# Optimization experiments

Hardware: AMD Instinct MI355X
Metric: run time of the kernel (lower is better)

Reference implementation:

```python
import jax, jax.numpy as jnp
import numpy as np

N = 400000   # active voxels
C = 64       # channels
G = 128      # voxel grid side
K = 27       # 3x3x3 kernel offsets
EPS = 1e-5   # BatchNorm eps


def _build_kernel_maps(rng):
    # random sparse 3D coordinates (unique voxels in a G^3 grid)
    lin = rng.choice(G ** 3, size=N, replace=False)
    coords = np.stack(np.unravel_index(lin, (G, G, G)), -1).astype(np.int64)  # [N,3]
    lut = np.full(G ** 3, N, dtype=np.int32)  # sentinel N = missing neighbor
    lut[lin] = np.arange(N, dtype=np.int32)
    offs = np.stack(np.meshgrid([-1, 0, 1], [-1, 0, 1], [-1, 0, 1], indexing='ij'), -1).reshape(-1, 3)  # [27,3]
    nbr = np.full((3, K, N), N, dtype=np.int32)
    for di, d in enumerate((1, 2, 3)):
        for k in range(K):
            nc = coords + offs[k] * d
            valid = np.all((nc >= 0) & (nc < G), axis=1)
            idx = np.ravel_multi_index(nc[valid].T, (G, G, G))
            nbr[di, k, valid] = lut[idx]
    return nbr


def setup_inputs() -> dict:
    key = jax.random.key(0)
    ks = jax.random.split(key, 20)
    rng = np.random.default_rng(0)
    nbr = jnp.asarray(_build_kernel_maps(rng))  # [3,27,N] int32
    s = 0.05
    inp = {
        'feats': jax.random.normal(ks[0], (N, C), jnp.float32),
        'nbr': nbr,
        # conv_init (dilation 1) + its BN
        'W_init': jax.random.normal(ks[1], (K, C, C), jnp.float32) * s,
        'b_init': jax.random.normal(ks[2], (C,), jnp.float32) * s,
        'g_init': jnp.ones((C,), jnp.float32),
        'be_init': jnp.zeros((C,), jnp.float32),
        'm_init': jax.random.normal(ks[3], (C,), jnp.float32) * s,
        'v_init': jax.random.uniform(ks[4], (C,), jnp.float32, 0.5, 1.5),
        # three branches (dilations 1,2,3), stacked on leading axis
        'W_br': jax.random.normal(ks[5], (3, K, C, C), jnp.float32) * s,
        'b_br': jax.random.normal(ks[6], (3, C), jnp.float32) * s,
        'g_br': jnp.ones((3, C), jnp.float32),
        'be_br': jnp.zeros((3, C), jnp.float32),
        'm_br': jax.random.normal(ks[7], (3, C), jnp.float32) * s,
        'v_br': jax.random.uniform(ks[8], (3, C), jnp.float32, 0.5, 1.5),
        # conv_out: 1x1 conv C -> 1
        'W_out': jax.random.normal(ks[9], (C, 1), jnp.float32) * s,
        'b_out': jax.random.normal(ks[10], (1,), jnp.float32) * s,
    }
    return inp


def _sparse_conv3(feats, nbr_k, W, b):
    # feats [N,C], nbr_k [27,N] (index N = missing), W [27,C,Cout], b [Cout]
    fpad = jnp.concatenate([feats, jnp.zeros((1, feats.shape[1]), feats.dtype)], 0)
    def step(acc, wn):
        Wk, nk = wn
        return acc + fpad[nk] @ Wk, None
    init = jnp.zeros((feats.shape[0], W.shape[-1]), feats.dtype) + b
    out, _ = jax.lax.scan(step, init, (W, nbr_k))
    return out


def _bn_relu(x, g, b, m, v):
    # inference-mode BatchNorm followed by ReLU
    return jax.nn.relu((x - m) * (g * jax.lax.rsqrt(v + EPS)) + b)


def reference(feats, nbr, W_init, b_init, g_init, be_init, m_init, v_init,
              W_br, b_br, g_br, be_br, m_br, v_br, W_out, b_out):
    x_init = _bn_relu(_sparse_conv3(feats, nbr[0], W_init, b_init),
                      g_init, be_init, m_init, v_init)
    def branch(W, b, g, be, m, v, nb):
        return _bn_relu(_sparse_conv3(x_init, nb, W, b), g, be, m, v)
    xb = jax.vmap(branch)(W_br, b_br, g_br, be_br, m_br, v_br, nbr)  # [3,N,C]
    x_fused = xb.sum(0) + x_init
    att = jax.nn.sigmoid(x_fused @ W_out + b_out)  # [N,1]
    return att
```

## Files before the change

### kernel.cpp

```cpp
#include <hip/hip_runtime.h>
#include <hip/hip_bf16.h>
#include <math.h>

#define NV 400000
#define ROWS_BLK 128
#define GRID_CONV 3125

typedef __bf16 bfv8 __attribute__((ext_vector_type(8)));
typedef float f32x4 __attribute__((ext_vector_type(4)));

#define GLOAD_LDS16(gp, lp) __builtin_amdgcn_global_load_lds(                 \
    (const __attribute__((address_space(1))) void*)(gp),                     \
    (__attribute__((address_space(3))) void*)(lp), 16, 0, 0)

__global__ void prep_feats_k(const float* __restrict__ feats,
                             __bf16* __restrict__ fpad,
                             __bf16* __restrict__ xpad)
{
    long t = (long)blockIdx.x * blockDim.x + threadIdx.x;
    long base = t * 4;
    const long nfeat = (long)NV * 64;
    const long total = (long)(NV + 1) * 64;
    if (base < total) {
        float x0 = 0.f, x1 = 0.f, x2 = 0.f, x3 = 0.f;
        if (base < nfeat) {
            const float4 v = *(const float4*)(feats + base);
            x0 = v.x; x1 = v.y; x2 = v.z; x3 = v.w;
        }
        union { __bf16 b[4]; ushort4 u; } pk;
        pk.b[0] = (__bf16)x0; pk.b[1] = (__bf16)x1;
        pk.b[2] = (__bf16)x2; pk.b[3] = (__bf16)x3;
        *(ushort4*)(fpad + base) = pk.u;
    }
    if (t < 64) xpad[(long)NV * 64 + t] = (__bf16)0.f;
}

__global__ void prep_w_k(const float* __restrict__ Winit,
                         const float* __restrict__ Wbr,
                         __bf16* __restrict__ wpk)
{
    int e = blockIdx.x * 256 + threadIdx.x;
    int i  = e & 7;
    int l  = (e >> 3) & 63;
    int cb = (e >> 9) & 3;
    int kc = (e >> 11) & 1;
    int kk = e >> 12;
    int k  = kk % 27;
    int s  = kk / 27;
    int cin  = kc * 32 + (l >> 4) * 8 + i;
    int cout = cb * 16 + (l & 15);
    float v = (s == 0) ? Winit[(k * 64 + cin) * 64 + cout]
                       : Wbr[(((s - 1) * 27 + k) * 64 + cin) * 64 + cout];
    wpk[e] = (__bf16)v;
}

__global__ void prep_bn_k(const float* __restrict__ b_init, const float* __restrict__ g_init,
                          const float* __restrict__ be_init, const float* __restrict__ m_init,
                          const float* __restrict__ v_init,
                          const float* __restrict__ b_br, const float* __restrict__ g_br,
                          const float* __restrict__ be_br, const float* __restrict__ m_br,
                          const float* __restrict__ v_br,
                          float* __restrict__ scale, float* __restrict__ shiftb)
{
    int t = threadIdx.x;
    int s = t >> 6, c = t & 63;
    float g, be, m, v, b;
    if (s == 0) { g = g_init[c]; be = be_init[c]; m = m_init[c]; v = v_init[c]; b = b_init[c]; }
    else { int o = (s - 1) * 64 + c; g = g_br[o]; be = be_br[o]; m = m_br[o]; v = v_br[o]; b = b_br[o]; }
    float sc = g / sqrtf(v + 1e-5f);
    scale[t]  = sc;
    shiftb[t] = (b - m) * sc + be;
}

struct Idx2 { int v[2]; };

__device__ __forceinline__ Idx2 load_idx(const int* __restrict__ nbr_t,
                                         long base, int l15)
{
    Idx2 r;
#pragma unroll
    for (int rg = 0; rg < 2; rg++) {
        long rr = base + rg * 16 + l15;
        r.v[rg] = nbr_t[rr];
    }
    return r;
}

__device__ __forceinline__ void stage_b(const __bf16* __restrict__ wtap,
                                        __bf16* lds_dst, int wid, int lane)
{
#pragma unroll
    for (int j = 0; j < 2; j++) {
        int chunk = wid * 2 + j;
        const __bf16* gp = wtap + chunk * 512 + lane * 8;
        __bf16* lp = lds_dst + chunk * 512;
        GLOAD_LDS16(gp, lp);
    }
}

__device__ __forceinline__ void issue_A(const __bf16* __restrict__ src,
                                        const Idx2 idx, int lg,
                                        bfv8 a0[2], bfv8 a1[2])
{
#pragma unroll
    for (int rg = 0; rg < 2; rg++) {
        const bfv8* ar = (const bfv8*)(src + (size_t)idx.v[rg] * 64);
        a0[rg] = ar[lg];
        a1[rg] = ar[4 + lg];
    }
}

__device__ __forceinline__ void mfma_tap(const __bf16* bbuf, int lane,
                                         const bfv8 a0[2], const bfv8 a1[2],
                                         f32x4 acc[2][4])
{
    const bfv8* wp = (const bfv8*)bbuf;
#pragma unroll
    for (int cb = 0; cb < 4; cb++) {
        bfv8 b0 = wp[cb * 64 + lane];
#pragma unroll
        for (int rg = 0; rg < 2; rg++)
            acc[rg][cb] = __builtin_amdgcn_mfma_f32_16x16x32_bf16(a0[rg], b0, acc[rg][cb], 0, 0, 0);
    }
#pragma unroll
    for (int cb = 0; cb < 4; cb++) {
        bfv8 b1 = wp[(4 + cb) * 64 + lane];
#pragma unroll
        for (int rg = 0; rg < 2; rg++)
            acc[rg][cb] = __builtin_amdgcn_mfma_f32_16x16x32_bf16(a1[rg], b1, acc[rg][cb], 0, 0, 0);
    }
}


__global__ __launch_bounds__(256, 4)
void conv_init_k(const __bf16* __restrict__ fpad, const int* __restrict__ nbr,
                 const __bf16* __restrict__ wpk, const float* __restrict__ scale,
                 const float* __restrict__ shiftb, const float* __restrict__ wout,
                 __bf16* __restrict__ xpad, float* __restrict__ logitpart)
{
    __shared__ __bf16 smem[4 * 4096];
    __bf16* tile = smem;
    const int tid = threadIdx.x;
    const int wid = tid >> 6, lane = tid & 63;
    const int l15 = lane & 15, lg = lane >> 4;
    const long base = (long)blockIdx.x * ROWS_BLK + wid * 32;

    f32x4 acc[2][4];
    f32x4 z = {0.f, 0.f, 0.f, 0.f};
#pragma unroll
    for (int a = 0; a < 2; a++)
#pragma unroll
        for (int b = 0; b < 4; b++) acc[a][b] = z;

    stage_b(wpk,                    smem + 0 * 4096, wid, lane);
    stage_b(wpk + (size_t)1 * 4096, smem + 1 * 4096, wid, lane);
    Idx2 i0 = load_idx(nbr,                  base, l15);
    Idx2 i1 = load_idx(nbr + (size_t)1 * NV, base, l15);
    Idx2 i2 = load_idx(nbr + (size_t)2 * NV, base, l15);
    __syncthreads();

    bfv8 aC0[2], aC1[2], aN0[2], aN1[2];
    issue_A(fpad, i0, lg, aC0, aC1);

#pragma unroll 2
    for (int k = 0; k < 25; k++) {
        issue_A(fpad, i1, lg, aN0, aN1);
        stage_b(wpk + (size_t)(k + 2) * 4096, smem + ((k + 2) & 3) * 4096, wid, lane);
        int tn = (k + 3 < 27) ? (k + 3) : 26;
        Idx2 inew = load_idx(nbr + (size_t)tn * NV, base, l15);
        asm volatile("s_waitcnt vmcnt(8)" ::: "memory");
        __builtin_amdgcn_s_barrier();
        __builtin_amdgcn_s_setprio(1);
        mfma_tap(smem + (k & 3) * 4096, lane, aC0, aC1, acc);
        __builtin_amdgcn_s_setprio(0);
#pragma unroll
        for (int rg = 0; rg < 2; rg++) { aC0[rg] = aN0[rg]; aC1[rg] = aN1[rg]; }
        i1 = i2; i2 = inew;
    }
    for (int k = 25; k < 27; k++) {
        if (k < 26) issue_A(fpad, i1, lg, aN0, aN1);
        __syncthreads();
        mfma_tap(smem + (k & 3) * 4096, lane, aC0, aC1, acc);
#pragma unroll
        for (int rg = 0; rg < 2; rg++) { aC0[rg] = aN0[rg]; aC1[rg] = aN1[rg]; }
        i1 = i2;
    }

    float sc[4], sh[4], wo[4];
#pragma unroll
    for (int cb = 0; cb < 4; cb++) {
        int col = cb * 16 + l15;
        sc[cb] = scale[col]; sh[cb] = shiftb[col]; wo[cb] = wout[col];
    }
    float lacc[2][4];
#pragma unroll
    for (int rg = 0; rg < 2; rg++)
#pragma unroll
        for (int j = 0; j < 4; j++) lacc[rg][j] = 0.f;

    __syncthreads();
#pragma unroll
    for (int rg = 0; rg < 2; rg++)
#pragma unroll
        for (int cb = 0; cb < 4; cb++)
#pragma unroll
            for (int j = 0; j < 4; j++) {
                float y = fmaxf(acc[rg][cb][j] * sc[cb] + sh[cb], 0.f);
                lacc[rg][j] += y * wo[cb];
                tile[(wid * 32 + rg * 16 + lg * 4 + j) * 64 + cb * 16 + l15] = (__bf16)y;
            }
    __syncthreads();

    {
        int r = tid >> 1, h = tid & 1;
        long grow = (long)blockIdx.x * ROWS_BLK + r;
        const f32x4* srcp = (const f32x4*)(tile + r * 64 + h * 32);
        f32x4* dst = (f32x4*)(xpad + grow * 64 + h * 32);
#pragma unroll
        for (int q = 0; q < 4; q++) dst[q] = srcp[q];
    }

#pragma unroll
    for (int rg = 0; rg < 2; rg++) {
        float red[4];
#pragma unroll
        for (int j = 0; j < 4; j++) {
            float t = lacc[rg][j];
            t += __shfl_xor(t, 1, 64);
            t += __shfl_xor(t, 2, 64);
            t += __shfl_xor(t, 4, 64);
            t += __shfl_xor(t, 8, 64);
            red[j] = t;
        }
        if (l15 == 0) {
            long row = base + rg * 16 + lg * 4;
            float4 o; o.x = red[0]; o.y = red[1]; o.z = red[2]; o.w = red[3];
            *(float4*)(logitpart + row) = o;
        }
    }
}

__global__ __launch_bounds__(256, 4)
void conv_br_k(const __bf16* __restrict__ xpad, const int* __restrict__ nbr,
               const __bf16* __restrict__ wpk, const float* __restrict__ scale,
               const float* __restrict__ shiftb, const float* __restrict__ wout,
               const float* __restrict__ bout, const float* __restrict__ logitpart,
               float* __restrict__ att)
{
    __shared__ __bf16 bbuf[4][4096];
    const int tid = threadIdx.x;
    const int wid = tid >> 6, lane = tid & 63;
    const int l15 = lane & 15, lg = lane >> 4;
    const long base = (long)blockIdx.x * ROWS_BLK + wid * 32;

    float wo[4];
#pragma unroll
    for (int cb = 0; cb < 4; cb++) wo[cb] = wout[cb * 16 + l15];

    float lacc[2][4];
#pragma unroll
    for (int rg = 0; rg < 2; rg++)
#pragma unroll
        for (int j = 0; j < 4; j++) lacc[rg][j] = 0.f;

    f32x4 acc[2][4];
    f32x4 z = {0.f, 0.f, 0.f, 0.f};
#pragma unroll
    for (int a = 0; a < 2; a++)
#pragma unroll
        for (int b = 0; b < 4; b++) acc[a][b] = z;

    auto do_epi = [&](int d) {
        float sc[4], sh[4];
#pragma unroll
        for (int cb = 0; cb < 4; cb++) {
            int col = (d + 1) * 64 + cb * 16 + l15;
            sc[cb] = scale[col]; sh[cb] = shiftb[col];
        }
#pragma unroll
        for (int rg = 0; rg < 2; rg++)
#pragma unroll
            for (int cb = 0; cb < 4; cb++)
#pragma unroll
                for (int j = 0; j < 4; j++) {
                    float y = fmaxf(acc[rg][cb][j] * sc[cb] + sh[cb], 0.f);
                    lacc[rg][j] += y * wo[cb];
                }
#pragma unroll
        for (int a = 0; a < 2; a++)
#pragma unroll
            for (int b = 0; b < 4; b++) acc[a][b] = z;
    };

    stage_b(wpk + (size_t)27 * 4096, bbuf[0], wid, lane);
    stage_b(wpk + (size_t)28 * 4096, bbuf[1], wid, lane);
    Idx2 i0 = load_idx(nbr,                  base, l15);
    Idx2 i1 = load_idx(nbr + (size_t)1 * NV, base, l15);
    Idx2 i2 = load_idx(nbr + (size_t)2 * NV, base, l15);
    __syncthreads();

    bfv8 aC0[2], aC1[2], aN0[2], aN1[2];
    issue_A(xpad, i0, lg, aC0, aC1);

#pragma unroll 2
    for (int k = 0; k < 79; k++) {
        issue_A(xpad, i1, lg, aN0, aN1);
        stage_b(wpk + (size_t)(k + 2 + 27) * 4096, bbuf[(k + 2) & 3], wid, lane);
        int tn = (k + 3 < 81) ? (k + 3) : 80;
        Idx2 inew = load_idx(nbr + (size_t)tn * NV, base, l15);
        asm volatile("s_waitcnt vmcnt(8)" ::: "memory");
        __builtin_amdgcn_s_barrier();
        __builtin_amdgcn_s_setprio(1);
        mfma_tap(bbuf[k & 3], lane, aC0, aC1, acc);
        __builtin_amdgcn_s_setprio(0);
        if (k == 26 || k == 53) do_epi(k / 27);
#pragma unroll
        for (int rg = 0; rg < 2; rg++) { aC0[rg] = aN0[rg]; aC1[rg] = aN1[rg]; }
        i1 = i2; i2 = inew;
    }
    for (int k = 79; k < 81; k++) {
        if (k < 80) issue_A(xpad, i1, lg, aN0, aN1);
        __syncthreads();
        mfma_tap(bbuf[k & 3], lane, aC0, aC1, acc);
#pragma unroll
        for (int rg = 0; rg < 2; rg++) { aC0[rg] = aN0[rg]; aC1[rg] = aN1[rg]; }
        i1 = i2;
    }
    do_epi(2);

    float bo = bout[0];
#pragma unroll
    for (int rg = 0; rg < 2; rg++) {
        float red[4];
#pragma unroll
        for (int j = 0; j < 4; j++) {
            float t = lacc[rg][j];
            t += __shfl_xor(t, 1, 64);
            t += __shfl_xor(t, 2, 64);
            t += __shfl_xor(t, 4, 64);
            t += __shfl_xor(t, 8, 64);
            red[j] = t;
        }
        if (l15 == 0) {
            long row = base + rg * 16 + lg * 4;
            float4 lp = *(const float4*)(logitpart + row);
            float4 o;
            o.x = 1.f / (1.f + expf(-(red[0] + lp.x + bo)));
            o.y = 1.f / (1.f + expf(-(red[1] + lp.y + bo)));
            o.z = 1.f / (1.f + expf(-(red[2] + lp.z + bo)));
            o.w = 1.f / (1.f + expf(-(red[3] + lp.w + bo)));
            *(float4*)(att + row) = o;
        }
    }
}

extern "C" void kernel_launch(void* const* d_in, const int* in_sizes, int n_in,
                              void* d_out, int out_size, void* d_ws, size_t ws_size,
                              hipStream_t stream)
{
    const float* feats  = (const float*)d_in[0];
    const int*   nbr    = (const int*)d_in[1];
    const float* W_init = (const float*)d_in[2];
    const float* b_init = (const float*)d_in[3];
    const float* g_init = (const float*)d_in[4];
    const float* be_init= (const float*)d_in[5];
    const float* m_init = (const float*)d_in[6];
    const float* v_init = (const float*)d_in[7];
    const float* W_br   = (const float*)d_in[8];
    const float* b_br   = (const float*)d_in[9];
    const float* g_br   = (const float*)d_in[10];
    const float* be_br  = (const float*)d_in[11];
    const float* m_br   = (const float*)d_in[12];
    const float* v_br   = (const float*)d_in[13];
    const float* W_out  = (const float*)d_in[14];
    const float* b_out  = (const float*)d_in[15];
    float* att = (float*)d_out;

    char* ws = (char*)d_ws;
    size_t off = 0;
    auto take = [&](size_t bytes) -> char* {
        char* p = ws + off;
        off = (off + bytes + 255) & ~(size_t)255;
        return p;
    };
    __bf16* fpad      = (__bf16*)take((size_t)(NV + 1) * 64 * 2);
    __bf16* xpad      = (__bf16*)take((size_t)(NV + 1) * 64 * 2);
    __bf16* wpk       = (__bf16*)take((size_t)4 * 27 * 4096 * 2);
    float*  scale     = (float*)take(4 * 64 * 4);
    float*  shiftb    = (float*)take(4 * 64 * 4);
    float*  logitpart = (float*)take((size_t)NV * 4);
    (void)in_sizes; (void)n_in; (void)out_size; (void)ws_size;

    prep_feats_k<<<25001, 256, 0, stream>>>(feats, fpad, xpad);
    prep_w_k<<<1728, 256, 0, stream>>>(W_init, W_br, wpk);
    prep_bn_k<<<1, 256, 0, stream>>>(b_init, g_init, be_init, m_init, v_init,
                                     b_br, g_br, be_br, m_br, v_br, scale, shiftb);
    conv_init_k<<<GRID_CONV, 256, 0, stream>>>(fpad, nbr, wpk, scale, shiftb,
                                               W_out, xpad, logitpart);
    conv_br_k<<<GRID_CONV, 256, 0, stream>>>(xpad, nbr, wpk, scale, shiftb,
                                             W_out, b_out, logitpart, att);
}
```

Before: 468.6 us.

## Deepen gather pipeline to two taps in flight with ping-pong A registers

Restructures both sparse-conv kernels so that gathered feature rows for two future taps are outstanding at once. The loop is manually unrolled by two and alternates between two register sets, and each new gather is issued right after the MFMA that consumes the old buffer, which removes the register copies. The BN scale/shift loads for all three branch epilogues are hoisted out of the loop into registers. The cost is higher register pressure, which could hurt occupancy under launch_bounds(256,4), and the waitcnt and barrier accounting now has to line up with deeper prefetch.

```diff
diff --git a/kernel.cpp b/kernel.cpp
--- a/kernel.cpp
+++ b/kernel.cpp
@@ -156,35 +156,48 @@
     stage_b(wpk + (size_t)1 * 4096, smem + 1 * 4096, wid, lane);
     Idx2 i0 = load_idx(nbr,                  base, l15);
     Idx2 i1 = load_idx(nbr + (size_t)1 * NV, base, l15);
-    Idx2 i2 = load_idx(nbr + (size_t)2 * NV, base, l15);
-    __syncthreads();
-
-    bfv8 aC0[2], aC1[2], aN0[2], aN1[2];
-    issue_A(fpad, i0, lg, aC0, aC1);
-
-#pragma unroll 2
-    for (int k = 0; k < 25; k++) {
-        issue_A(fpad, i1, lg, aN0, aN1);
-        stage_b(wpk + (size_t)(k + 2) * 4096, smem + ((k + 2) & 3) * 4096, wid, lane);
-        int tn = (k + 3 < 27) ? (k + 3) : 26;
-        Idx2 inew = load_idx(nbr + (size_t)tn * NV, base, l15);
-        asm volatile("s_waitcnt vmcnt(8)" ::: "memory");
-        __builtin_amdgcn_s_barrier();
-        __builtin_amdgcn_s_setprio(1);
-        mfma_tap(smem + (k & 3) * 4096, lane, aC0, aC1, acc);
-        __builtin_amdgcn_s_setprio(0);
-#pragma unroll
-        for (int rg = 0; rg < 2; rg++) { aC0[rg] = aN0[rg]; aC1[rg] = aN1[rg]; }
-        i1 = i2; i2 = inew;
-    }
-    for (int k = 25; k < 27; k++) {
-        if (k < 26) issue_A(fpad, i1, lg, aN0, aN1);
-        __syncthreads();
-        mfma_tap(smem + (k & 3) * 4096, lane, aC0, aC1, acc);
-#pragma unroll
-        for (int rg = 0; rg < 2; rg++) { aC0[rg] = aN0[rg]; aC1[rg] = aN1[rg]; }
-        i1 = i2;
-    }
+    Idx2 iA = load_idx(nbr + (size_t)2 * NV, base, l15);
+    Idx2 iB = load_idx(nbr + (size_t)3 * NV, base, l15);
+    bfv8 aX0[2], aX1[2], aY0[2], aY1[2];
+    issue_A(fpad, i0, lg, aX0, aX1);
+    issue_A(fpad, i1, lg, aY0, aY1);
+    __syncthreads();
+
+    for (int kb = 0; kb < 12; kb++) {
+        {
+            int k = 2 * kb;
+            asm volatile("s_waitcnt vmcnt(8)" ::: "memory");
+            __builtin_amdgcn_s_barrier();
+            __builtin_amdgcn_s_setprio(1);
+            mfma_tap(smem + (k & 3) * 4096, lane, aX0, aX1, acc);
+            __builtin_amdgcn_s_setprio(0);
+            issue_A(fpad, iA, lg, aX0, aX1);
+            stage_b(wpk + (size_t)(k + 2) * 4096, smem + ((k + 2) & 3) * 4096, wid, lane);
+            int tn = (k + 4 < 27) ? (k + 4) : 26;
+            Idx2 nw = load_idx(nbr + (size_t)tn * NV, base, l15);
+            iA = iB; iB = nw;
+        }
+        {
+            int k = 2 * kb + 1;
+            asm volatile("s_waitcnt vmcnt(8)" ::: "memory");
+            __builtin_amdgcn_s_barrier();
+            __builtin_amdgcn_s_setprio(1);
+            mfma_tap(smem + (k & 3) * 4096, lane, aY0, aY1, acc);
+            __builtin_amdgcn_s_setprio(0);
+            issue_A(fpad, iA, lg, aY0, aY1);
+            stage_b(wpk + (size_t)(k + 2) * 4096, smem + ((k + 2) & 3) * 4096, wid, lane);
+            int tn = (k + 4 < 27) ? (k + 4) : 26;
+            Idx2 nw = load_idx(nbr + (size_t)tn * NV, base, l15);
+            iA = iB; iB = nw;
+        }
+    }
+    __syncthreads();
+    mfma_tap(smem + 0 * 4096, lane, aX0, aX1, acc);
+    mfma_tap(smem + 1 * 4096, lane, aY0, aY1, acc);
+    stage_b(wpk + (size_t)26 * 4096, smem + 2 * 4096, wid, lane);
+    issue_A(fpad, iA, lg, aX0, aX1);
+    __syncthreads();
+    mfma_tap(smem + 2 * 4096, lane, aX0, aX1, acc);
 
     float sc[4], sh[4], wo[4];
 #pragma unroll
@@ -252,10 +265,18 @@
     const int wid = tid >> 6, lane = tid & 63;
     const int l15 = lane & 15, lg = lane >> 4;
     const long base = (long)blockIdx.x * ROWS_BLK + wid * 32;
-
-    float wo[4];
-#pragma unroll
-    for (int cb = 0; cb < 4; cb++) wo[cb] = wout[cb * 16 + l15];
+    const __bf16* wsrc = wpk + (size_t)27 * 4096;
+
+    float wo[4], esc[3][4], esh[3][4];
+#pragma unroll
+    for (int cb = 0; cb < 4; cb++) {
+        wo[cb] = wout[cb * 16 + l15];
+#pragma unroll
+        for (int d = 0; d < 3; d++) {
+            int col = (d + 1) * 64 + cb * 16 + l15;
+            esc[d][cb] = scale[col]; esh[d][cb] = shiftb[col];
+        }
+    }
 
     float lacc[2][4];
 #pragma unroll
@@ -271,19 +292,13 @@
         for (int b = 0; b < 4; b++) acc[a][b] = z;
 
     auto do_epi = [&](int d) {
-        float sc[4], sh[4];
-#pragma unroll
-        for (int cb = 0; cb < 4; cb++) {
-            int col = (d + 1) * 64 + cb * 16 + l15;
-            sc[cb] = scale[col]; sh[cb] = shiftb[col];
-        }
 #pragma unroll
         for (int rg = 0; rg < 2; rg++)
 #pragma unroll
             for (int cb = 0; cb < 4; cb++)
 #pragma unroll
                 for (int j = 0; j < 4; j++) {
-                    float y = fmaxf(acc[rg][cb][j] * sc[cb] + sh[cb], 0.f);
+                    float y = fmaxf(acc[rg][cb][j] * esc[d][cb] + esh[d][cb], 0.f);
                     lacc[rg][j] += y * wo[cb];
                 }
 #pragma unroll
@@ -292,40 +307,54 @@
             for (int b = 0; b < 4; b++) acc[a][b] = z;
     };
 
-    stage_b(wpk + (size_t)27 * 4096, bbuf[0], wid, lane);
-    stage_b(wpk + (size_t)28 * 4096, bbuf[1], wid, lane);
+    stage_b(wsrc,                    bbuf[0], wid, lane);
+    stage_b(wsrc + (size_t)1 * 4096, bbuf[1], wid, lane);
     Idx2 i0 = load_idx(nbr,                  base, l15);
     Idx2 i1 = load_idx(nbr + (size_t)1 * NV, base, l15);
-    Idx2 i2 = load_idx(nbr + (size_t)2 * NV, base, l15);
-    __syncthreads();
-
-    bfv8 aC0[2], aC1[2], aN0[2], aN1[2];
-    issue_A(xpad, i0, lg, aC0, aC1);
-
-#pragma unroll 2
-    for (int k = 0; k < 79; k++) {
-        issue_A(xpad, i1, lg, aN0, aN1);
-        stage_b(wpk + (size_t)(k + 2 + 27) * 4096, bbuf[(k + 2) & 3], wid, lane);
-        int tn = (k + 3 < 81) ? (k + 3) : 80;
-        Idx2 inew = load_idx(nbr + (size_t)tn * NV, base, l15);
-        asm volatile("s_waitcnt vmcnt(8)" ::: "memory");
-        __builtin_amdgcn_s_barrier();
-        __builtin_amdgcn_s_setprio(1);
-        mfma_tap(bbuf[k & 3], lane, aC0, aC1, acc);
-        __builtin_amdgcn_s_setprio(0);
-        if (k == 26 || k == 53) do_epi(k / 27);
-#pragma unroll
-        for (int rg = 0; rg < 2; rg++) { aC0[rg] = aN0[rg]; aC1[rg] = aN1[rg]; }
-        i1 = i2; i2 = inew;
-    }
-    for (int k = 79; k < 81; k++) {
-        if (k < 80) issue_A(xpad, i1, lg, aN0, aN1);
-        __syncthreads();
-        mfma_tap(bbuf[k & 3], lane, aC0, aC1, acc);
-#pragma unroll
-        for (int rg = 0; rg < 2; rg++) { aC0[rg] = aN0[rg]; aC1[rg] = aN1[rg]; }
-        i1 = i2;
-    }
+    Idx2 iA = load_idx(nbr + (size_t)2 * NV, base, l15);
+    Idx2 iB = load_idx(nbr + (size_t)3 * NV, base, l15);
+    bfv8 aX0[2], aX1[2], aY0[2], aY1[2];
+    issue_A(xpad, i0, lg, aX0, aX1);
+    issue_A(xpad, i1, lg, aY0, aY1);
+    __syncthreads();
+
+    for (int kb = 0; kb < 39; kb++) {
+        {
+            int k = 2 * kb;
+            asm volatile("s_waitcnt vmcnt(8)" ::: "memory");
+            __builtin_amdgcn_s_barrier();
+            __builtin_amdgcn_s_setprio(1);
+            mfma_tap(bbuf[k & 3], lane, aX0, aX1, acc);
+            __builtin_amdgcn_s_setprio(0);
+            if (k == 26) do_epi(0);
+            issue_A(xpad, iA, lg, aX0, aX1);
+            stage_b(wsrc + (size_t)(k + 2) * 4096, bbuf[(k + 2) & 3], wid, lane);
+            int tn = (k + 4 < 81) ? (k + 4) : 80;
+            Idx2 nw = load_idx(nbr + (size_t)tn * NV, base, l15);
+            iA = iB; iB = nw;
+        }
+        {
+            int k = 2 * kb + 1;
+            asm volatile("s_waitcnt vmcnt(8)" ::: "memory");
+            __builtin_amdgcn_s_barrier();
+            __builtin_amdgcn_s_setprio(1);
+            mfma_tap(bbuf[k & 3], lane, aY0, aY1, acc);
+            __builtin_amdgcn_s_setprio(0);
+            if (k == 53) do_epi(1);
+            issue_A(xpad, iA, lg, aY0, aY1);
+            stage_b(wsrc + (size_t)(k + 2) * 4096, bbuf[(k + 2) & 3], wid, lane);
+            int tn = (k + 4 < 81) ? (k + 4) : 80;
+            Idx2 nw = load_idx(nbr + (size_t)tn * NV, base, l15);
+            iA = iB; iB = nw;
+        }
+    }
+    __syncthreads();
+    mfma_tap(bbuf[2], lane, aX0, aX1, acc);
+    mfma_tap(bbuf[3], lane, aY0, aY1, acc);
+    stage_b(wsrc + (size_t)80 * 4096, bbuf[0], wid, lane);
+    issue_A(xpad, iA, lg, aX0, aX1);
+    __syncthreads();
+    mfma_tap(bbuf[0], lane, aX0, aX1, acc);
     do_epi(2);
 
     float bo = bout[0];
```

Result: slower. 482.1 us (+2.9%).
